# Kernel tuning notes

Measured on AMD Instinct MI355X. Metric: run time of the kernel, lower is better.

The kernel has to match this reference:

```python
import jax, jax.numpy as jnp
import numpy as np

GCN_DIM, GEO_DIM, HIDDEN_DIM, TOWER_DIM, RECENT_K = 128, 32, 256, 128, 50
NUM_ITEMS, NUM_USERS = 100000, 16384


def _normalize(x, eps=1e-12):
    # torch F.normalize(dim=1): x / max(||x||, eps)
    n = jnp.linalg.norm(x, axis=1, keepdims=True)
    return x / jnp.maximum(n, eps)


def setup_inputs() -> dict:
    key = jax.random.key(0)
    ks = jax.random.split(key, 16)
    s = 0.05  # weight init scale
    return {
        "item_feat": jax.random.normal(ks[0], (NUM_ITEMS, 2), jnp.float32),
        "gcn_item_emb": jax.random.normal(ks[1], (NUM_ITEMS, GCN_DIM), jnp.float32),
        "gcn_user_emb": jax.random.normal(ks[2], (NUM_USERS, GCN_DIM), jnp.float32),
        "user_items": jax.random.randint(ks[3], (NUM_USERS, RECENT_K), 0, NUM_ITEMS, jnp.int32),
        "Wg": s * jax.random.normal(ks[4], (2, GEO_DIM), jnp.float32),
        "bg": jnp.zeros((GEO_DIM,), jnp.float32),
        "Wi1": s * jax.random.normal(ks[5], (GCN_DIM + GEO_DIM, HIDDEN_DIM), jnp.float32),
        "bi1": jnp.zeros((HIDDEN_DIM,), jnp.float32),
        "Wi2": s * jax.random.normal(ks[6], (HIDDEN_DIM, TOWER_DIM), jnp.float32),
        "bi2": jnp.zeros((TOWER_DIM,), jnp.float32),
        "Wq": s * jax.random.normal(ks[7], (GCN_DIM, TOWER_DIM), jnp.float32),
        "bq": jnp.zeros((TOWER_DIM,), jnp.float32),
        "Wk": s * jax.random.normal(ks[8], (TOWER_DIM, TOWER_DIM), jnp.float32),
        "bk": jnp.zeros((TOWER_DIM,), jnp.float32),
        "Wu1": s * jax.random.normal(ks[9], (GCN_DIM + TOWER_DIM, HIDDEN_DIM), jnp.float32),
        "bu1": jnp.zeros((HIDDEN_DIM,), jnp.float32),
        "Wu2": s * jax.random.normal(ks[10], (HIDDEN_DIM, TOWER_DIM), jnp.float32),
        "bu2": jnp.zeros((TOWER_DIM,), jnp.float32),
    }


def reference(item_feat, gcn_item_emb, gcn_user_emb, user_items,
              Wg, bg, Wi1, bi1, Wi2, bi2, Wq, bq, Wk, bk, Wu1, bu1, Wu2, bu2):
    # ---- encode_items ----
    geo = jax.nn.relu(item_feat @ Wg + bg)                       # [I, GEO]
    xi = jnp.concatenate([geo, gcn_item_emb], axis=1)            # [I, GEO+GCN]
    item_emb = _normalize(jax.nn.relu(xi @ Wi1 + bi1) @ Wi2 + bi2)  # [I, T]

    # ---- encode_users (batched ragged attention pooling) ----
    h = item_emb[user_items]                                     # [U, K, T] gather
    q = gcn_user_emb @ Wq + bq                                   # [U, T]
    k = h @ Wk + bk                                              # [U, K, T]
    scores = jnp.einsum('ut,ukt->uk', q, k)                      # [U, K]
    alpha = jax.nn.softmax(scores, axis=1)                       # softmax over history
    rep = jnp.einsum('uk,ukt->ut', alpha, h)                     # [U, T]
    fused = jnp.concatenate([gcn_user_emb, rep], axis=1)         # [U, GCN+T]
    user_emb = _normalize(jax.nn.relu(fused @ Wu1 + bu1) @ Wu2 + bu2)  # [U, T]

    return jnp.concatenate([item_emb, user_emb], axis=0)         # [I+U, T]
```

## Files before the change

kernel.cpp:

```cpp
#include <hip/hip_runtime.h>
#include <hip/hip_bf16.h>
#include <math.h>

#define NITEMS 100000
#define NUSERS 16384
#define GCN 128
#define GEO 32
#define HIDD 256
#define TD 128
#define RK 50

typedef unsigned int uint;
typedef unsigned short ushort;
typedef __bf16 bf16x8 __attribute__((ext_vector_type(8)));
typedef float f32x4 __attribute__((ext_vector_type(4)));

__device__ __forceinline__ ushort bfb(float x) {
  union { __hip_bfloat16 b; ushort u; } t; t.b = __float2bfloat16(x); return t.u;
}
__device__ __forceinline__ uint packbf2(float a, float b) {
  return (uint)bfb(a) | ((uint)bfb(b) << 16);
}
__device__ __forceinline__ float bflo(uint d) { return __uint_as_float(d << 16); }
__device__ __forceinline__ float bfhi(uint d) { return __uint_as_float(d & 0xffff0000u); }

union U4B { uint4 u; bf16x8 b; };
__device__ __forceinline__ bf16x8 ldfrag(const ushort* p) { U4B t; t.u = *(const uint4*)p; return t.b; }

__global__ __launch_bounds__(256) void prep_convert(
    const float* __restrict__ Wi1, const float* __restrict__ Wi2,
    const float* __restrict__ Wu1, const float* __restrict__ Wu2,
    ushort* __restrict__ Wi1P, ushort* __restrict__ Wi2P,
    ushort* __restrict__ Wu1P, ushort* __restrict__ Wu2P)
{
  int id = blockIdx.x * 256 + threadIdx.x;
  if (id < 40960) {
    int k = id >> 8, c = id & 255;
    Wi1P[(k >> 5) * 8192 + c * 32 + (k & 31)] = bfb(Wi1[id]);
  } else if (id < 73728) {
    int i = id - 40960; int k = i >> 7, c = i & 127;
    Wi2P[(k >> 5) * 4096 + c * 32 + (k & 31)] = bfb(Wi2[i]);
  } else if (id < 139264) {
    int i = id - 73728; int k = i >> 8, c = i & 255;
    Wu1P[(k >> 5) * 8192 + c * 32 + (k & 31)] = bfb(Wu1[i]);
  } else if (id < 172032) {
    int i = id - 139264; int k = i >> 7, c = i & 127;
    Wu2P[(k >> 5) * 4096 + c * 32 + (k & 31)] = bfb(Wu2[i]);
  }
}

__global__ __launch_bounds__(256) void prep_wqk(
    const float* __restrict__ Wq, const float* __restrict__ Wk,
    const float* __restrict__ bq, float* __restrict__ WqkS, float* __restrict__ bqk)
{
  int id = blockIdx.x * 256 + threadIdx.x;
  if (id < 16384) {
    int g = id >> 7, s = id & 127;
    float acc = 0.f;
    for (int t = 0; t < 128; ++t) acc = fmaf(Wq[g * 128 + t], Wk[s * 128 + t], acc);
    WqkS[g * 128 + s] = acc;
  } else if (id < 16512) {
    int s = id - 16384;
    float acc = 0.f;
    for (int t = 0; t < 128; ++t) acc = fmaf(bq[t], Wk[s * 128 + t], acc);
    bqk[s] = acc;
  }
}

template <int K1, bool ITEM>
__global__ __launch_bounds__(256, 4) void mlp_kernel(
    const float* __restrict__ xmain,
    const float* __restrict__ feat,
    const float* __restrict__ Wg, const float* __restrict__ bg,
    const ushort* __restrict__ repB,
    const ushort* __restrict__ W1P, const float* __restrict__ b1,
    const ushort* __restrict__ W2P, const float* __restrict__ b2,
    float* __restrict__ outp, ushort* __restrict__ outb, int M)
{
  constexpr int ASTR = ITEM ? 168 : 264;
  constexpr int K1CH = K1 / 32;
  __shared__ __align__(16) ushort s_a[64 * 264];
  __shared__ float s_red[64 * 4];
  __shared__ float s_inv[64];

  const int tid = threadIdx.x;
  const int wid = tid >> 6, lane = tid & 63, g = lane >> 4, q = lane & 15;
  const int i0 = blockIdx.x * 64;

  if (ITEM) {
    #pragma unroll
    for (int r = 0; r < 8; ++r) {
      int lin = r * 256 + tid;
      int it = lin >> 5, c4 = (lin & 31) * 4;
      int row = i0 + it;
      float4 v = make_float4(0.f, 0.f, 0.f, 0.f);
      if (row < M) v = *(const float4*)(xmain + (size_t)row * GCN + c4);
      *(uint*)(&s_a[it * ASTR + GEO + c4])     = packbf2(v.x, v.y);
      *(uint*)(&s_a[it * ASTR + GEO + c4 + 2]) = packbf2(v.z, v.w);
    }
    #pragma unroll
    for (int r = 0; r < 8; ++r) {
      int lin = r * 256 + tid;
      int it = lin >> 5, gg = lin & 31;
      int row = i0 + it;
      float f0 = 0.f, f1 = 0.f;
      if (row < M) { f0 = feat[(size_t)row * 2]; f1 = feat[(size_t)row * 2 + 1]; }
      s_a[it * ASTR + gg] = bfb(fmaxf(fmaf(f0, Wg[gg], fmaf(f1, Wg[GEO + gg], bg[gg])), 0.f));
    }
  } else {
    #pragma unroll
    for (int r = 0; r < 8; ++r) {
      int lin = r * 256 + tid;
      int it = lin >> 5, c4 = (lin & 31) * 4;
      float4 v = *(const float4*)(xmain + (size_t)(i0 + it) * GCN + c4);
      *(uint*)(&s_a[it * ASTR + c4])     = packbf2(v.x, v.y);
      *(uint*)(&s_a[it * ASTR + c4 + 2]) = packbf2(v.z, v.w);
    }
    #pragma unroll
    for (int r = 0; r < 4; ++r) {
      int lin = r * 256 + tid;
      int it = lin >> 4, c8 = (lin & 15) * 8;
      *(uint4*)(&s_a[it * ASTR + GCN + c8]) = *(const uint4*)(repB + (size_t)(i0 + it) * TD + c8);
    }
  }
  __syncthreads();

  f32x4 acc[4][4];
  #pragma unroll
  for (int cf = 0; cf < 4; ++cf) {
    float bv = b1[wid * 64 + cf * 16 + q];
    f32x4 t = {bv, bv, bv, bv};
    #pragma unroll
    for (int rf = 0; rf < 4; ++rf) acc[rf][cf] = t;
  }
  {
    const ushort* bbase = W1P + (wid * 64 + q) * 32 + g * 8;
    #pragma unroll
    for (int kb = 0; kb < K1CH; ++kb) {
      bf16x8 af[4], bfr[4];
      #pragma unroll
      for (int rf = 0; rf < 4; ++rf) af[rf] = ldfrag(&s_a[(16 * rf + q) * ASTR + kb * 32 + g * 8]);
      #pragma unroll
      for (int cf = 0; cf < 4; ++cf) bfr[cf] = ldfrag(bbase + kb * 8192 + cf * 512);
      #pragma unroll
      for (int rf = 0; rf < 4; ++rf)
        #pragma unroll
        for (int cf = 0; cf < 4; ++cf)
          acc[rf][cf] = __builtin_amdgcn_mfma_f32_16x16x32_bf16(af[rf], bfr[cf], acc[rf][cf], 0, 0, 0);
    }
  }
  __syncthreads();

  #pragma unroll
  for (int rf = 0; rf < 4; ++rf)
    #pragma unroll
    for (int cf = 0; cf < 4; ++cf)
      #pragma unroll
      for (int e = 0; e < 4; ++e) {
        float v = fmaxf(acc[rf][cf][e], 0.f);
        float vp = __shfl_xor(v, 1);
        if (!(q & 1))
          *(uint*)(&s_a[(16 * rf + 4 * g + e) * 264 + wid * 64 + cf * 16 + q]) = packbf2(v, vp);
      }
  __syncthreads();

  f32x4 acc2[4][2];
  #pragma unroll
  for (int cf = 0; cf < 2; ++cf) {
    float bv = b2[wid * 32 + cf * 16 + q];
    f32x4 t = {bv, bv, bv, bv};
    #pragma unroll
    for (int rf = 0; rf < 4; ++rf) acc2[rf][cf] = t;
  }
  {
    const ushort* bbase = W2P + (wid * 32 + q) * 32 + g * 8;
    #pragma unroll
    for (int kb = 0; kb < 8; ++kb) {
      bf16x8 af[4], bf2[2];
      #pragma unroll
      for (int rf = 0; rf < 4; ++rf) af[rf] = ldfrag(&s_a[(16 * rf + q) * 264 + kb * 32 + g * 8]);
      #pragma unroll
      for (int cf = 0; cf < 2; ++cf) bf2[cf] = ldfrag(bbase + kb * 4096 + cf * 512);
      #pragma unroll
      for (int rf = 0; rf < 4; ++rf)
        #pragma unroll
        for (int cf = 0; cf < 2; ++cf)
          acc2[rf][cf] = __builtin_amdgcn_mfma_f32_16x16x32_bf16(af[rf], bf2[cf], acc2[rf][cf], 0, 0, 0);
    }
  }

  #pragma unroll
  for (int rf = 0; rf < 4; ++rf) {
    #pragma unroll
    for (int e = 0; e < 4; ++e) {
      float p = acc2[rf][0][e] * acc2[rf][0][e] + acc2[rf][1][e] * acc2[rf][1][e];
      p += __shfl_xor(p, 1, 16); p += __shfl_xor(p, 2, 16);
      p += __shfl_xor(p, 4, 16); p += __shfl_xor(p, 8, 16);
      if (q == 0) s_red[(16 * rf + 4 * g + e) * 4 + wid] = p;
    }
  }
  __syncthreads();
  if (tid < 64) {
    float s = s_red[tid * 4] + s_red[tid * 4 + 1] + s_red[tid * 4 + 2] + s_red[tid * 4 + 3];
    s_inv[tid] = 1.f / fmaxf(sqrtf(s), 1e-12f);
  }
  __syncthreads();

  #pragma unroll
  for (int rf = 0; rf < 4; ++rf) {
    #pragma unroll
    for (int e = 0; e < 4; ++e) {
      int row = 16 * rf + 4 * g + e;
      int grow = i0 + row;
      if (grow < M) {
        float sc = s_inv[row];
        #pragma unroll
        for (int cf = 0; cf < 2; ++cf) {
          float v = acc2[rf][cf][e] * sc;
          outp[(size_t)grow * TD + wid * 32 + cf * 16 + q] = v;
          if (ITEM) outb[(size_t)grow * TD + wid * 32 + cf * 16 + q] = bfb(v);
        }
      }
    }
  }
}

__global__ __launch_bounds__(256) void qt_kernel(
    const float* __restrict__ gcn_user, const float* __restrict__ WqkS,
    const float* __restrict__ bqk, float* __restrict__ qt)
{
  __shared__ float s_gue[16 * 132];
  const int tid = threadIdx.x;
  const int u0 = blockIdx.x * 16;
  #pragma unroll
  for (int r = 0; r < 8; ++r) {
    int lin = r * 256 + tid;
    int u = lin >> 7, c = lin & 127;
    s_gue[u * 132 + c] = gcn_user[(size_t)(u0 + u) * GCN + c];
  }
  __syncthreads();
  const int ul = tid >> 4, tx = tid & 15, c0 = tx * 8;
  float a[8];
  { float4 b4 = *(const float4*)(bqk + c0); float4 b5 = *(const float4*)(bqk + c0 + 4);
    a[0]=b4.x; a[1]=b4.y; a[2]=b4.z; a[3]=b4.w; a[4]=b5.x; a[5]=b5.y; a[6]=b5.z; a[7]=b5.w; }
  for (int g = 0; g < 128; ++g) {
    float x = s_gue[ul * 132 + g];
    float4 w4 = *(const float4*)(WqkS + g * 128 + c0);
    float4 w5 = *(const float4*)(WqkS + g * 128 + c0 + 4);
    a[0] = fmaf(x, w4.x, a[0]); a[1] = fmaf(x, w4.y, a[1]);
    a[2] = fmaf(x, w4.z, a[2]); a[3] = fmaf(x, w4.w, a[3]);
    a[4] = fmaf(x, w5.x, a[4]); a[5] = fmaf(x, w5.y, a[5]);
    a[6] = fmaf(x, w5.z, a[6]); a[7] = fmaf(x, w5.w, a[7]);
  }
  float* op = qt + (size_t)(u0 + ul) * TD + c0;
  *(float4*)op = make_float4(a[0], a[1], a[2], a[3]);
  *(float4*)(op + 4) = make_float4(a[4], a[5], a[6], a[7]);
}

__global__ __launch_bounds__(256) void attn_kernel(
    const int* __restrict__ user_items, const float* __restrict__ qt,
    const ushort* __restrict__ itemB, ushort* __restrict__ repB)
{
  __shared__ int s_idx[4][52];
  const int tid = threadIdx.x;
  const int wid = tid >> 6, lane = tid & 63, g = lane >> 4, q = lane & 15;
  const int u = blockIdx.x * 4 + wid;
  const int c0 = q * 8;

  if (lane < 52) s_idx[wid][lane] = (lane < 50) ? user_items[(size_t)u * RK + lane] : 0;
  float qv[8];
  { float4 a = *(const float4*)(qt + (size_t)u * TD + c0);
    float4 b = *(const float4*)(qt + (size_t)u * TD + c0 + 4);
    qv[0]=a.x; qv[1]=a.y; qv[2]=a.z; qv[3]=a.w; qv[4]=b.x; qv[5]=b.y; qv[6]=b.z; qv[7]=b.w; }
  __syncthreads();

  uint4 h[13]; float sc[13];
  #pragma unroll
  for (int i = 0; i < 13; ++i) {
    int j = 4 * i + g;
    int idx = s_idx[wid][j];
    h[i] = *(const uint4*)(itemB + (size_t)idx * TD + c0);
    float p = bflo(h[i].x) * qv[0] + bfhi(h[i].x) * qv[1]
            + bflo(h[i].y) * qv[2] + bfhi(h[i].y) * qv[3]
            + bflo(h[i].z) * qv[4] + bfhi(h[i].z) * qv[5]
            + bflo(h[i].w) * qv[6] + bfhi(h[i].w) * qv[7];
    p += __shfl_xor(p, 1, 16); p += __shfl_xor(p, 2, 16);
    p += __shfl_xor(p, 4, 16); p += __shfl_xor(p, 8, 16);
    sc[i] = (j < RK) ? p : -3.0e38f;
  }
  float m = sc[0];
  #pragma unroll
  for (int i = 1; i < 13; ++i) m = fmaxf(m, sc[i]);
  m = fmaxf(m, __shfl_xor(m, 16, 64));
  m = fmaxf(m, __shfl_xor(m, 32, 64));
  float ssum = 0.f;
  #pragma unroll
  for (int i = 0; i < 13; ++i) { sc[i] = __expf(sc[i] - m); ssum += sc[i]; }
  ssum += __shfl_xor(ssum, 16, 64);
  ssum += __shfl_xor(ssum, 32, 64);
  const float inv = 1.f / ssum;
  float rep[8] = {0, 0, 0, 0, 0, 0, 0, 0};
  #pragma unroll
  for (int i = 0; i < 13; ++i) {
    float a = sc[i] * inv;
    rep[0] = fmaf(a, bflo(h[i].x), rep[0]); rep[1] = fmaf(a, bfhi(h[i].x), rep[1]);
    rep[2] = fmaf(a, bflo(h[i].y), rep[2]); rep[3] = fmaf(a, bfhi(h[i].y), rep[3]);
    rep[4] = fmaf(a, bflo(h[i].z), rep[4]); rep[5] = fmaf(a, bfhi(h[i].z), rep[5]);
    rep[6] = fmaf(a, bflo(h[i].w), rep[6]); rep[7] = fmaf(a, bfhi(h[i].w), rep[7]);
  }
  #pragma unroll
  for (int c = 0; c < 8; ++c) {
    rep[c] += __shfl_xor(rep[c], 16, 64);
    rep[c] += __shfl_xor(rep[c], 32, 64);
  }
  if (g == 0) {
    uint4 o;
    o.x = packbf2(rep[0], rep[1]); o.y = packbf2(rep[2], rep[3]);
    o.z = packbf2(rep[4], rep[5]); o.w = packbf2(rep[6], rep[7]);
    *(uint4*)(repB + (size_t)u * TD + c0) = o;
  }
}

extern "C" void kernel_launch(void* const* d_in, const int* in_sizes, int n_in,
                              void* d_out, int out_size, void* d_ws, size_t ws_size,
                              hipStream_t stream) {
  const float* item_feat  = (const float*)d_in[0];
  const float* gcn_item   = (const float*)d_in[1];
  const float* gcn_user   = (const float*)d_in[2];
  const int*   user_items = (const int*)  d_in[3];
  const float* Wg  = (const float*)d_in[4];
  const float* bg  = (const float*)d_in[5];
  const float* Wi1 = (const float*)d_in[6];
  const float* bi1 = (const float*)d_in[7];
  const float* Wi2 = (const float*)d_in[8];
  const float* bi2 = (const float*)d_in[9];
  const float* Wq  = (const float*)d_in[10];
  const float* bq  = (const float*)d_in[11];
  const float* Wk  = (const float*)d_in[12];
  const float* Wu1 = (const float*)d_in[14];
  const float* bu1 = (const float*)d_in[15];
  const float* Wu2 = (const float*)d_in[16];
  const float* bu2 = (const float*)d_in[17];
  float* out = (float*)d_out;

  char* ws = (char*)d_ws;
  ushort* Wi1P  = (ushort*)(ws + 0);
  ushort* Wi2P  = (ushort*)(ws + 81920);
  ushort* Wu1P  = (ushort*)(ws + 147456);
  ushort* Wu2P  = (ushort*)(ws + 278528);
  float*  WqkS  = (float*) (ws + 344064);
  float*  bqk   = (float*) (ws + 409600);
  float*  qtb   = (float*) (ws + 410112);
  ushort* itemB = (ushort*)(ws + 8798720);
  ushort* repB  = (ushort*)(ws + 34398720);

  prep_convert<<<672, 256, 0, stream>>>(Wi1, Wi2, Wu1, Wu2, Wi1P, Wi2P, Wu1P, Wu2P);
  prep_wqk<<<65, 256, 0, stream>>>(Wq, Wk, bq, WqkS, bqk);
  qt_kernel<<<NUSERS / 16, 256, 0, stream>>>(gcn_user, WqkS, bqk, qtb);
  mlp_kernel<160, true><<<(NITEMS + 63) / 64, 256, 0, stream>>>(
      gcn_item, item_feat, Wg, bg, nullptr, Wi1P, bi1, Wi2P, bi2, out, itemB, NITEMS);
  attn_kernel<<<NUSERS / 4, 256, 0, stream>>>(user_items, qtb, itemB, repB);
  mlp_kernel<256, false><<<NUSERS / 64, 256, 0, stream>>>(
      gcn_user, nullptr, Wg, bg, repB, Wu1P, bu1, Wu2P, bu2, out + (size_t)NITEMS * TD, nullptr, NUSERS);
}
```

Before: 144.5 us.

## Prefetch MLP weight fragments, shrink user MLP tile, vectorize Wqk prep

The MLP kernel now loads the next k-block's weight fragments from global memory while the current block's MFMAs run, and loads the first fragments before the input staging. The kernel is templated on row count, and the user MLP now uses 32-row tiles so it launches more blocks. Launch bounds drop from 4 to 3 blocks per CU, which allows more registers for the prefetch buffers at the cost of occupancy. Other changes: prep_wqk uses float4 loads, the hidden activation is written to shared memory as 16-bit stores instead of shuffle-packed 32-bit stores, and a __syncthreads in attn_kernel is removed because each wave only reads the indices it wrote itself.

New measurement: 137.6 us. 4.8% less time.

```diff
diff --git a/kernel.cpp b/kernel.cpp
--- a/kernel.cpp
+++ b/kernel.cpp
@@ -57,18 +57,26 @@
   if (id < 16384) {
     int g = id >> 7, s = id & 127;
     float acc = 0.f;
-    for (int t = 0; t < 128; ++t) acc = fmaf(Wq[g * 128 + t], Wk[s * 128 + t], acc);
+    for (int t = 0; t < 128; t += 4) {
+      float4 a = *(const float4*)(Wq + g * 128 + t);
+      float4 b = *(const float4*)(Wk + s * 128 + t);
+      acc += a.x * b.x + a.y * b.y + a.z * b.z + a.w * b.w;
+    }
     WqkS[g * 128 + s] = acc;
   } else if (id < 16512) {
     int s = id - 16384;
     float acc = 0.f;
-    for (int t = 0; t < 128; ++t) acc = fmaf(bq[t], Wk[s * 128 + t], acc);
+    for (int t = 0; t < 128; t += 4) {
+      float4 a = *(const float4*)(bq + t);
+      float4 b = *(const float4*)(Wk + s * 128 + t);
+      acc += a.x * b.x + a.y * b.y + a.z * b.z + a.w * b.w;
+    }
     bqk[s] = acc;
   }
 }
 
-template <int K1, bool ITEM>
-__global__ __launch_bounds__(256, 4) void mlp_kernel(
+template <int ROWS, int K1, bool ITEM>
+__global__ __launch_bounds__(256, 3) void mlp_kernel(
     const float* __restrict__ xmain,
     const float* __restrict__ feat,
     const float* __restrict__ Wg, const float* __restrict__ bg,
@@ -77,19 +85,25 @@
     const ushort* __restrict__ W2P, const float* __restrict__ b2,
     float* __restrict__ outp, ushort* __restrict__ outb, int M)
 {
+  constexpr int RF = ROWS / 16;
+  constexpr int K1CH = K1 / 32;
   constexpr int ASTR = ITEM ? 168 : 264;
-  constexpr int K1CH = K1 / 32;
-  __shared__ __align__(16) ushort s_a[64 * 264];
-  __shared__ float s_red[64 * 4];
-  __shared__ float s_inv[64];
+  __shared__ __align__(16) ushort s_a[ROWS * 264];
+  __shared__ float s_red[ROWS * 4];
+  __shared__ float s_inv[ROWS];
 
   const int tid = threadIdx.x;
   const int wid = tid >> 6, lane = tid & 63, g = lane >> 4, q = lane & 15;
-  const int i0 = blockIdx.x * 64;
-
-  if (ITEM) {
-    #pragma unroll
-    for (int r = 0; r < 8; ++r) {
+  const int i0 = blockIdx.x * ROWS;
+
+  const ushort* bbase1 = W1P + (wid * 64 + q) * 32 + g * 8;
+  bf16x8 bcur[4];
+  #pragma unroll
+  for (int cf = 0; cf < 4; ++cf) bcur[cf] = ldfrag(bbase1 + cf * 512);
+
+  if constexpr (ITEM) {
+    #pragma unroll
+    for (int r = 0; r < ROWS / 8; ++r) {
       int lin = r * 256 + tid;
       int it = lin >> 5, c4 = (lin & 31) * 4;
       int row = i0 + it;
@@ -99,7 +113,7 @@
       *(uint*)(&s_a[it * ASTR + GEO + c4 + 2]) = packbf2(v.z, v.w);
     }
     #pragma unroll
-    for (int r = 0; r < 8; ++r) {
+    for (int r = 0; r < ROWS / 8; ++r) {
       int lin = r * 256 + tid;
       int it = lin >> 5, gg = lin & 31;
       int row = i0 + it;
@@ -109,7 +123,7 @@
     }
   } else {
     #pragma unroll
-    for (int r = 0; r < 8; ++r) {
+    for (int r = 0; r < ROWS / 8; ++r) {
       int lin = r * 256 + tid;
       int it = lin >> 5, c4 = (lin & 31) * 4;
       float4 v = *(const float4*)(xmain + (size_t)(i0 + it) * GCN + c4);
@@ -117,7 +131,7 @@
       *(uint*)(&s_a[it * ASTR + c4 + 2]) = packbf2(v.z, v.w);
     }
     #pragma unroll
-    for (int r = 0; r < 4; ++r) {
+    for (int r = 0; r < ROWS / 16; ++r) {
       int lin = r * 256 + tid;
       int it = lin >> 4, c8 = (lin & 15) * 8;
       *(uint4*)(&s_a[it * ASTR + GCN + c8]) = *(const uint4*)(repB + (size_t)(i0 + it) * TD + c8);
@@ -125,72 +139,82 @@
   }
   __syncthreads();
 
-  f32x4 acc[4][4];
+  f32x4 acc[RF][4];
   #pragma unroll
   for (int cf = 0; cf < 4; ++cf) {
     float bv = b1[wid * 64 + cf * 16 + q];
     f32x4 t = {bv, bv, bv, bv};
     #pragma unroll
-    for (int rf = 0; rf < 4; ++rf) acc[rf][cf] = t;
-  }
-  {
-    const ushort* bbase = W1P + (wid * 64 + q) * 32 + g * 8;
-    #pragma unroll
-    for (int kb = 0; kb < K1CH; ++kb) {
-      bf16x8 af[4], bfr[4];
-      #pragma unroll
-      for (int rf = 0; rf < 4; ++rf) af[rf] = ldfrag(&s_a[(16 * rf + q) * ASTR + kb * 32 + g * 8]);
-      #pragma unroll
-      for (int cf = 0; cf < 4; ++cf) bfr[cf] = ldfrag(bbase + kb * 8192 + cf * 512);
-      #pragma unroll
-      for (int rf = 0; rf < 4; ++rf)
-        #pragma unroll
-        for (int cf = 0; cf < 4; ++cf)
-          acc[rf][cf] = __builtin_amdgcn_mfma_f32_16x16x32_bf16(af[rf], bfr[cf], acc[rf][cf], 0, 0, 0);
-    }
-  }
-  __syncthreads();
-
-  #pragma unroll
-  for (int rf = 0; rf < 4; ++rf)
+    for (int rf = 0; rf < RF; ++rf) acc[rf][cf] = t;
+  }
+  #pragma unroll
+  for (int kb = 0; kb < K1CH; ++kb) {
+    bf16x8 bnxt[4];
+    if (kb + 1 < K1CH) {
+      #pragma unroll
+      for (int cf = 0; cf < 4; ++cf) bnxt[cf] = ldfrag(bbase1 + (kb + 1) * 8192 + cf * 512);
+    }
+    bf16x8 af[RF];
+    #pragma unroll
+    for (int rf = 0; rf < RF; ++rf) af[rf] = ldfrag(&s_a[(16 * rf + q) * ASTR + kb * 32 + g * 8]);
+    #pragma unroll
+    for (int rf = 0; rf < RF; ++rf)
+      #pragma unroll
+      for (int cf = 0; cf < 4; ++cf)
+        acc[rf][cf] = __builtin_amdgcn_mfma_f32_16x16x32_bf16(af[rf], bcur[cf], acc[rf][cf], 0, 0, 0);
+    if (kb + 1 < K1CH) {
+      #pragma unroll
+      for (int cf = 0; cf < 4; ++cf) bcur[cf] = bnxt[cf];
+    }
+  }
+
+  const ushort* bbase2 = W2P + (wid * 32 + q) * 32 + g * 8;
+  bf16x8 b2cur[2];
+  #pragma unroll
+  for (int cf = 0; cf < 2; ++cf) b2cur[cf] = ldfrag(bbase2 + cf * 512);
+
+  __syncthreads();
+
+  #pragma unroll
+  for (int rf = 0; rf < RF; ++rf)
     #pragma unroll
     for (int cf = 0; cf < 4; ++cf)
       #pragma unroll
-      for (int e = 0; e < 4; ++e) {
-        float v = fmaxf(acc[rf][cf][e], 0.f);
-        float vp = __shfl_xor(v, 1);
-        if (!(q & 1))
-          *(uint*)(&s_a[(16 * rf + 4 * g + e) * 264 + wid * 64 + cf * 16 + q]) = packbf2(v, vp);
-      }
-  __syncthreads();
-
-  f32x4 acc2[4][2];
+      for (int e = 0; e < 4; ++e)
+        s_a[(16 * rf + 4 * g + e) * 264 + wid * 64 + cf * 16 + q] = bfb(fmaxf(acc[rf][cf][e], 0.f));
+  __syncthreads();
+
+  f32x4 acc2[RF][2];
   #pragma unroll
   for (int cf = 0; cf < 2; ++cf) {
     float bv = b2[wid * 32 + cf * 16 + q];
     f32x4 t = {bv, bv, bv, bv};
     #pragma unroll
-    for (int rf = 0; rf < 4; ++rf) acc2[rf][cf] = t;
-  }
-  {
-    const ushort* bbase = W2P + (wid * 32 + q) * 32 + g * 8;
-    #pragma unroll
-    for (int kb = 0; kb < 8; ++kb) {
-      bf16x8 af[4], bf2[2];
-      #pragma unroll
-      for (int rf = 0; rf < 4; ++rf) af[rf] = ldfrag(&s_a[(16 * rf + q) * 264 + kb * 32 + g * 8]);
-      #pragma unroll
-      for (int cf = 0; cf < 2; ++cf) bf2[cf] = ldfrag(bbase + kb * 4096 + cf * 512);
-      #pragma unroll
-      for (int rf = 0; rf < 4; ++rf)
-        #pragma unroll
-        for (int cf = 0; cf < 2; ++cf)
-          acc2[rf][cf] = __builtin_amdgcn_mfma_f32_16x16x32_bf16(af[rf], bf2[cf], acc2[rf][cf], 0, 0, 0);
-    }
-  }
-
-  #pragma unroll
-  for (int rf = 0; rf < 4; ++rf) {
+    for (int rf = 0; rf < RF; ++rf) acc2[rf][cf] = t;
+  }
+  #pragma unroll
+  for (int kb = 0; kb < 8; ++kb) {
+    bf16x8 bnxt[2];
+    if (kb < 7) {
+      #pragma unroll
+      for (int cf = 0; cf < 2; ++cf) bnxt[cf] = ldfrag(bbase2 + (kb + 1) * 4096 + cf * 512);
+    }
+    bf16x8 af[RF];
+    #pragma unroll
+    for (int rf = 0; rf < RF; ++rf) af[rf] = ldfrag(&s_a[(16 * rf + q) * 264 + kb * 32 + g * 8]);
+    #pragma unroll
+    for (int rf = 0; rf < RF; ++rf)
+      #pragma unroll
+      for (int cf = 0; cf < 2; ++cf)
+        acc2[rf][cf] = __builtin_amdgcn_mfma_f32_16x16x32_bf16(af[rf], b2cur[cf], acc2[rf][cf], 0, 0, 0);
+    if (kb < 7) {
+      #pragma unroll
+      for (int cf = 0; cf < 2; ++cf) b2cur[cf] = bnxt[cf];
+    }
+  }
+
+  #pragma unroll
+  for (int rf = 0; rf < RF; ++rf) {
     #pragma unroll
     for (int e = 0; e < 4; ++e) {
       float p = acc2[rf][0][e] * acc2[rf][0][e] + acc2[rf][1][e] * acc2[rf][1][e];
@@ -200,14 +224,14 @@
     }
   }
   __syncthreads();
-  if (tid < 64) {
+  if (tid < ROWS) {
     float s = s_red[tid * 4] + s_red[tid * 4 + 1] + s_red[tid * 4 + 2] + s_red[tid * 4 + 3];
     s_inv[tid] = 1.f / fmaxf(sqrtf(s), 1e-12f);
   }
   __syncthreads();
 
   #pragma unroll
-  for (int rf = 0; rf < 4; ++rf) {
+  for (int rf = 0; rf < RF; ++rf) {
     #pragma unroll
     for (int e = 0; e < 4; ++e) {
       int row = 16 * rf + 4 * g + e;
@@ -218,7 +242,7 @@
         for (int cf = 0; cf < 2; ++cf) {
           float v = acc2[rf][cf][e] * sc;
           outp[(size_t)grow * TD + wid * 32 + cf * 16 + q] = v;
-          if (ITEM) outb[(size_t)grow * TD + wid * 32 + cf * 16 + q] = bfb(v);
+          if constexpr (ITEM) outb[(size_t)grow * TD + wid * 32 + cf * 16 + q] = bfb(v);
         }
       }
     }
@@ -272,7 +296,6 @@
   { float4 a = *(const float4*)(qt + (size_t)u * TD + c0);
     float4 b = *(const float4*)(qt + (size_t)u * TD + c0 + 4);
     qv[0]=a.x; qv[1]=a.y; qv[2]=a.z; qv[3]=a.w; qv[4]=b.x; qv[5]=b.y; qv[6]=b.z; qv[7]=b.w; }
-  __syncthreads();
 
   uint4 h[13]; float sc[13];
   #pragma unroll
@@ -357,9 +380,9 @@
   prep_convert<<<672, 256, 0, stream>>>(Wi1, Wi2, Wu1, Wu2, Wi1P, Wi2P, Wu1P, Wu2P);
   prep_wqk<<<65, 256, 0, stream>>>(Wq, Wk, bq, WqkS, bqk);
   qt_kernel<<<NUSERS / 16, 256, 0, stream>>>(gcn_user, WqkS, bqk, qtb);
-  mlp_kernel<160, true><<<(NITEMS + 63) / 64, 256, 0, stream>>>(
+  mlp_kernel<64, 160, true><<<(NITEMS + 63) / 64, 256, 0, stream>>>(
       gcn_item, item_feat, Wg, bg, nullptr, Wi1P, bi1, Wi2P, bi2, out, itemB, NITEMS);
   attn_kernel<<<NUSERS / 4, 256, 0, stream>>>(user_items, qtb, itemB, repB);
-  mlp_kernel<256, false><<<NUSERS / 64, 256, 0, stream>>>(
+  mlp_kernel<32, 256, false><<<NUSERS / 32, 256, 0, stream>>>(
       gcn_user, nullptr, Wg, bg, repB, Wu1P, bu1, Wu2P, bu2, out + (size_t)NITEMS * TD, nullptr, NUSERS);
 }
```
